# Performance work log

Hardware: AMD Instinct MI355X
Metric: run time of the kernel (lower is better)

Reference implementation:

```python
import jax, jax.numpy as jnp
import numpy as np

B, S, D_MODEL, D_STATE = 4, 2048, 2048, 64
C = 8.0
SURPRISE_TEMP = 1.0
RMS_EPS = 1e-6


def _l2norm(x, eps=1e-12):
    # F.normalize(dim=-1): x / max(||x||_2, eps)
    n = jnp.sqrt(jnp.sum(x * x, axis=-1, keepdims=True))
    return x / jnp.maximum(n, eps)


def setup_inputs() -> dict:
    key = jax.random.key(0)
    ks = jax.random.split(key, 9)
    std = 0.02
    return {
        "x": jax.random.normal(ks[0], (B, S, D_MODEL), dtype=jnp.float32),
        "Wk": jax.random.normal(ks[1], (D_STATE, D_MODEL), dtype=jnp.float32) * std,
        "Wv": jax.random.normal(ks[2], (D_STATE, D_MODEL), dtype=jnp.float32) * std,
        "Wq": jax.random.normal(ks[3], (D_STATE, D_MODEL), dtype=jnp.float32) * std,
        "Wa_w": jax.random.normal(ks[4], (D_STATE, D_MODEL), dtype=jnp.float32) * std,
        "Wa_b": jnp.zeros((D_STATE,), dtype=jnp.float32),
        "lam": jax.random.uniform(ks[5], (D_STATE,), dtype=jnp.float32, minval=4.0, maxval=9.0),
        "norm_w": jnp.ones((D_STATE,), dtype=jnp.float32),
        "Wo": jax.random.normal(ks[6], (D_MODEL, D_STATE), dtype=jnp.float32) * std,
    }


def reference(x, Wk, Wv, Wq, Wa_w, Wa_b, lam, norm_w, Wo):
    b, s, _ = x.shape
    d = Wk.shape[0]
    # projections
    k = _l2norm(x @ Wk.T)                    # [B,S,d]
    v = x @ Wv.T                             # [B,S,d]
    q = _l2norm(x @ Wq.T)                    # [B,S,d]
    r = jax.nn.sigmoid(x @ Wa_w.T + Wa_b)    # [B,S,d]
    log_a = jnp.log(jax.nn.sigmoid(lam) + 1e-8)
    alpha = jnp.exp(C * r * log_a)           # [B,S,d]

    def step(H, inp):
        # H: [B, d_k, d_v]; inp tensors: [B, d]
        k_t, v_t, q_t, a_t = inp
        pred = jnp.einsum("bk,bkv->bv", q_t, H)
        err = jnp.sum((v_t - pred) ** 2, axis=-1, keepdims=True)   # [B,1]
        surprise = jax.nn.sigmoid(err / (SURPRISE_TEMP + 1e-6))    # [B,1]
        kH = jnp.einsum("bk,bkv->bv", k_t, H)
        # delta = k (x) v - k (x) (k^T H) = k (x) (v - kH)
        delta = k_t[:, :, None] * (v_t - kH)[:, None, :]           # [B,d,d]
        a = a_t[:, :, None]                                        # gate over k-dim rows
        H = a * H + (1.0 - a) * (surprise[:, :, None] * delta)
        y_t = jnp.einsum("bk,bkv->bv", q_t, H)
        return H, y_t

    H0 = jnp.zeros((b, d, d), dtype=x.dtype)
    xs = (
        jnp.swapaxes(k, 0, 1),
        jnp.swapaxes(v, 0, 1),
        jnp.swapaxes(q, 0, 1),
        jnp.swapaxes(alpha, 0, 1),
    )
    _, ys = jax.lax.scan(step, H0, xs)       # ys: [S,B,d]
    y = jnp.swapaxes(ys, 0, 1)               # [B,S,d]

    # RMSNorm (computed in fp32, cast back)
    yf = y.astype(jnp.float32)
    yn = yf * jax.lax.rsqrt(jnp.mean(yf * yf, axis=-1, keepdims=True) + RMS_EPS)
    yn = (yn * norm_w).astype(y.dtype)

    return yn @ Wo.T                          # [B,S,d_model]
```

## Files before the change

kernel.cpp:

```cpp
#include <hip/hip_runtime.h>
#include <hip/hip_bf16.h>
#include <math.h>

#define B_ 4
#define S_ 2048
#define DM_ 2048

__device__ __forceinline__ float wave_reduce_add_f32(float x) {
  float t;
  t = __int_as_float(__builtin_amdgcn_update_dpp(0, __float_as_int(x), 0x111, 0xf, 0xf, true)); x += t;
  t = __int_as_float(__builtin_amdgcn_update_dpp(0, __float_as_int(x), 0x112, 0xf, 0xf, true)); x += t;
  t = __int_as_float(__builtin_amdgcn_update_dpp(0, __float_as_int(x), 0x114, 0xf, 0xf, true)); x += t;
  t = __int_as_float(__builtin_amdgcn_update_dpp(0, __float_as_int(x), 0x118, 0xf, 0xf, true)); x += t;
  t = __int_as_float(__builtin_amdgcn_update_dpp(0, __float_as_int(x), 0x142, 0xa, 0xf, true)); x += t;
  t = __int_as_float(__builtin_amdgcn_update_dpp(0, __float_as_int(x), 0x143, 0xc, 0xf, true)); x += t;
  return __int_as_float(__builtin_amdgcn_readlane(__float_as_int(x), 63));
}

__global__ __launch_bounds__(256) void k_proj(
    const float* __restrict__ x, const float* __restrict__ Wk,
    const float* __restrict__ Wv, const float* __restrict__ Wq,
    const float* __restrict__ Wa, const float* __restrict__ Wab,
    const float* __restrict__ lam, float* __restrict__ proj)
{
  __shared__ __align__(16) float xs[16 * 40];
  __shared__ __align__(16) float ws[32 * 260];
  const int tid = threadIdx.x;
  const int r0  = blockIdx.x * 16;
  const int ct  = tid & 63;
  const int rt  = tid >> 6;
  float acc[4][4];
  #pragma unroll
  for (int r = 0; r < 4; r++) { acc[r][0] = 0.f; acc[r][1] = 0.f; acc[r][2] = 0.f; acc[r][3] = 0.f; }

  const int sg = tid >> 3;
  const int sm = tid & 7;
  const float* wbase[4] = {Wk, Wv, Wq, Wa};

  for (int k0 = 0; k0 < DM_; k0 += 32) {
    if (tid < 128) {
      const int rr = tid >> 3;
      const int ko = (tid & 7) << 2;
      float4 xv = *(const float4*)(x + (size_t)(r0 + rr) * DM_ + k0 + ko);
      *(float4*)(xs + rr * 40 + ko) = xv;
    }
    #pragma unroll
    for (int p = 0; p < 8; p++) {
      const int c = sg + p * 32;
      const float* wb = wbase[p >> 1];
      const int cc = c - (p >> 1) * 64;
      float4 wv = *(const float4*)(wb + (size_t)cc * DM_ + k0 + sm * 4);
      ws[(sm * 4 + 0) * 260 + c] = wv.x;
      ws[(sm * 4 + 1) * 260 + c] = wv.y;
      ws[(sm * 4 + 2) * 260 + c] = wv.z;
      ws[(sm * 4 + 3) * 260 + c] = wv.w;
    }
    __syncthreads();
    #pragma unroll
    for (int kq = 0; kq < 8; kq++) {
      float4 xv[4];
      #pragma unroll
      for (int r = 0; r < 4; r++) xv[r] = *(const float4*)(xs + (rt * 4 + r) * 40 + kq * 4);
      #pragma unroll
      for (int i = 0; i < 4; i++) {
        const int kk = kq * 4 + i;
        float wv0 = ws[kk * 260 + ct];
        float wv1 = ws[kk * 260 + ct + 64];
        float wv2 = ws[kk * 260 + ct + 128];
        float wv3 = ws[kk * 260 + ct + 192];
        #pragma unroll
        for (int r = 0; r < 4; r++) {
          float xr = (i == 0) ? xv[r].x : (i == 1) ? xv[r].y : (i == 2) ? xv[r].z : xv[r].w;
          acc[r][0] = fmaf(xr, wv0, acc[r][0]);
          acc[r][1] = fmaf(xr, wv1, acc[r][1]);
          acc[r][2] = fmaf(xr, wv2, acc[r][2]);
          acc[r][3] = fmaf(xr, wv3, acc[r][3]);
        }
      }
    }
    __syncthreads();
  }
  float lamv = lam[ct];
  float la = logf(1.f / (1.f + expf(-lamv)) + 1e-8f);
  float bv = Wab[ct];
  #pragma unroll
  for (int r = 0; r < 4; r++) {
    float nk = wave_reduce_add_f32(acc[r][0] * acc[r][0]);
    float nq = wave_reduce_add_f32(acc[r][2] * acc[r][2]);
    nk = fmaxf(sqrtf(nk), 1e-12f);
    nq = fmaxf(sqrtf(nq), 1e-12f);
    float pre = acc[r][3] + bv;
    float rr_ = 1.f / (1.f + expf(-pre));
    float al  = expf(8.f * rr_ * la);
    float* pr = proj + (size_t)(r0 + rt * 4 + r) * 256;
    pr[ct]        = acc[r][0] / nk;
    pr[64 + ct]   = acc[r][1];
    pr[128 + ct]  = acc[r][2] / nq;
    pr[192 + ct]  = al;
  }
}

__global__ __launch_bounds__(256) void k_scan(const float* __restrict__ proj,
                                              float* __restrict__ ypart)
{
  __shared__ __align__(16) float inv[2][256];
  __shared__ __align__(16) float red[2][2][4][64];
  const int b    = blockIdx.x;
  const int tid  = threadIdx.x;
  const int w    = tid >> 6;
  const int lane = tid & 63;
  const int kb   = w * 16;
  float H[16];
  #pragma unroll
  for (int j = 0; j < 16; j++) H[j] = 0.f;
  const float* pb = proj + (size_t)b * S_ * 256;
  float* yb = ypart + (size_t)b * S_ * 256;
  float pf0 = pb[tid];
  float pf1 = pb[256 + tid];
  for (int t = 0; t < S_; t++) {
    const int pp = t & 1;
    inv[pp][tid] = pf0;
    pf0 = pf1;
    pf1 = (t + 2 < S_) ? pb[(size_t)(t + 2) * 256 + tid] : 0.f;
    __syncthreads();
    float k_[16], q_[16], a_[16];
    #pragma unroll
    for (int jq = 0; jq < 4; jq++) {
      *(float4*)(k_ + jq * 4) = *(const float4*)(&inv[pp][kb + jq * 4]);
      *(float4*)(q_ + jq * 4) = *(const float4*)(&inv[pp][128 + kb + jq * 4]);
      *(float4*)(a_ + jq * 4) = *(const float4*)(&inv[pp][192 + kb + jq * 4]);
    }
    float vv = inv[pp][64 + lane];
    float pred_p = 0.f, kH_p = 0.f;
    #pragma unroll
    for (int j = 0; j < 16; j++) {
      pred_p = fmaf(q_[j], H[j], pred_p);
      kH_p   = fmaf(k_[j], H[j], kH_p);
    }
    red[pp][0][w][lane] = pred_p;
    red[pp][1][w][lane] = kH_p;
    __syncthreads();
    float pred = (red[pp][0][0][lane] + red[pp][0][1][lane]) + (red[pp][0][2][lane] + red[pp][0][3][lane]);
    float kH   = (red[pp][1][0][lane] + red[pp][1][1][lane]) + (red[pp][1][2][lane] + red[pp][1][3][lane]);
    float d = vv - pred;
    float e = wave_reduce_add_f32(d * d);
    float s = 1.f / (1.f + expf(-e * (1.f / 1.000001f)));
    float g = s * (vv - kH);
    float yp = 0.f;
    #pragma unroll
    for (int j = 0; j < 16; j++) {
      H[j] = fmaf(a_[j], H[j], (1.f - a_[j]) * k_[j] * g);
      yp = fmaf(q_[j], H[j], yp);
    }
    yb[(size_t)t * 256 + w * 64 + lane] = yp;
  }
}

__global__ __launch_bounds__(256) void k_trans(const float* __restrict__ Wo,
                                               float* __restrict__ WoT) {
  int i = blockIdx.x * 256 + threadIdx.x;
  int d = i >> 11;
  int c = i & 2047;
  WoT[i] = Wo[(size_t)c * 64 + d];
}

__global__ __launch_bounds__(256) void k_out(const float* __restrict__ ypart,
    const float* __restrict__ norm_w, const float* __restrict__ WoT,
    float* __restrict__ out)
{
  __shared__ __align__(16) float yn[16 * 64];
  const int tid = threadIdx.x;
  const int r0  = blockIdx.x * 16;
  const int c0  = blockIdx.y * 512;
  {
    const int r = tid >> 4;
    const int d = (tid & 15) * 4;
    const float* yp = ypart + (size_t)(r0 + r) * 256;
    float4 y0 = *(const float4*)(yp + d);
    float4 y1 = *(const float4*)(yp + 64 + d);
    float4 y2 = *(const float4*)(yp + 128 + d);
    float4 y3 = *(const float4*)(yp + 192 + d);
    float yx = y0.x + y1.x + y2.x + y3.x;
    float yy = y0.y + y1.y + y2.y + y3.y;
    float yz = y0.z + y1.z + y2.z + y3.z;
    float yw = y0.w + y1.w + y2.w + y3.w;
    float sq = yx * yx + yy * yy + yz * yz + yw * yw;
    sq += __shfl_xor(sq, 1, 64);
    sq += __shfl_xor(sq, 2, 64);
    sq += __shfl_xor(sq, 4, 64);
    sq += __shfl_xor(sq, 8, 64);
    float rms = rsqrtf(sq * (1.f / 64.f) + 1e-6f);
    float4 nw = *(const float4*)(norm_w + d);
    yn[r * 64 + d + 0] = yx * rms * nw.x;
    yn[r * 64 + d + 1] = yy * rms * nw.y;
    yn[r * 64 + d + 2] = yz * rms * nw.z;
    yn[r * 64 + d + 3] = yw * rms * nw.w;
  }
  __syncthreads();
  const int ctq = tid & 127;
  const int rt  = tid >> 7;
  float acc[8][4];
  #pragma unroll
  for (int r = 0; r < 8; r++) { acc[r][0] = 0.f; acc[r][1] = 0.f; acc[r][2] = 0.f; acc[r][3] = 0.f; }
  #pragma unroll 8
  for (int d = 0; d < 64; d++) {
    float4 wv = *(const float4*)(WoT + (size_t)d * 2048 + c0 + ctq * 4);
    #pragma unroll
    for (int r = 0; r < 8; r++) {
      float yv = yn[(rt * 8 + r) * 64 + d];
      acc[r][0] = fmaf(yv, wv.x, acc[r][0]);
      acc[r][1] = fmaf(yv, wv.y, acc[r][1]);
      acc[r][2] = fmaf(yv, wv.z, acc[r][2]);
      acc[r][3] = fmaf(yv, wv.w, acc[r][3]);
    }
  }
  #pragma unroll
  for (int r = 0; r < 8; r++) {
    float4 o; o.x = acc[r][0]; o.y = acc[r][1]; o.z = acc[r][2]; o.w = acc[r][3];
    *(float4*)(out + (size_t)(r0 + rt * 8 + r) * 2048 + c0 + ctq * 4) = o;
  }
}

extern "C" void kernel_launch(void* const* d_in, const int* in_sizes, int n_in,
                              void* d_out, int out_size, void* d_ws, size_t ws_size,
                              hipStream_t stream) {
  const float* x   = (const float*)d_in[0];
  const float* Wk  = (const float*)d_in[1];
  const float* Wv  = (const float*)d_in[2];
  const float* Wq  = (const float*)d_in[3];
  const float* Wa  = (const float*)d_in[4];
  const float* Wab = (const float*)d_in[5];
  const float* lam = (const float*)d_in[6];
  const float* nw  = (const float*)d_in[7];
  const float* Wo  = (const float*)d_in[8];
  float* out = (float*)d_out;

  float* wsf   = (float*)d_ws;
  float* proj  = wsf;
  float* ypart = wsf + 2097152;
  float* WoT   = wsf + 4194304;

  k_trans<<<dim3(512), dim3(256), 0, stream>>>(Wo, WoT);
  k_proj <<<dim3(512), dim3(256), 0, stream>>>(x, Wk, Wv, Wq, Wa, Wab, lam, proj);
  k_scan <<<dim3(4),   dim3(256), 0, stream>>>(proj, ypart);
  k_out  <<<dim3(512, 4), dim3(256), 0, stream>>>(ypart, nw, WoT, out);
}
```

Measured before the change: 1.440 ms.

## Prefetch scan inputs directly into registers and drop one barrier per step

The scan kernel now loads each timestep's k, q, alpha, (1-alpha)*k and v straight from global memory into registers, two steps ahead with a ping-pong register set. This removes the shared-memory staging buffer and one __syncthreads per step. The projection kernel precomputes (1-alpha)*k into a wider row stride, and the reduction uses a transposed shared layout so each lane reads its partials with a single float4 load, plus a raw s_barrier and a fast reciprocal/exp. The cost is more register pressure, a larger workspace and redundant global loads of the same row across waves.

Measured after the change: 1.911 ms. 32.7% more time.

```diff
diff --git a/kernel.cpp b/kernel.cpp
--- a/kernel.cpp
+++ b/kernel.cpp
@@ -5,6 +5,7 @@
 #define B_ 4
 #define S_ 2048
 #define DM_ 2048
+#define PROJ_STRIDE 320
 
 __device__ __forceinline__ float wave_reduce_add_f32(float x) {
   float t;
@@ -92,67 +93,87 @@
     float pre = acc[r][3] + bv;
     float rr_ = 1.f / (1.f + expf(-pre));
     float al  = expf(8.f * rr_ * la);
-    float* pr = proj + (size_t)(r0 + rt * 4 + r) * 256;
-    pr[ct]        = acc[r][0] / nk;
+    float kn  = acc[r][0] / nk;
+    float* pr = proj + (size_t)(r0 + rt * 4 + r) * PROJ_STRIDE;
+    pr[ct]        = kn;
     pr[64 + ct]   = acc[r][1];
     pr[128 + ct]  = acc[r][2] / nq;
     pr[192 + ct]  = al;
-  }
+    pr[256 + ct]  = (1.f - al) * kn;
+  }
+}
+
+__device__ __forceinline__ void load_row(const float* __restrict__ r,
+    float4 K[4], float4 Q[4], float4 A[4], float4 W[4], float& V,
+    int w, int lane) {
+  const float4* r4 = (const float4*)r;
+  const int o = w * 4;
+  #pragma unroll
+  for (int i = 0; i < 4; i++) {
+    K[i] = r4[o + i];
+    Q[i] = r4[32 + o + i];
+    A[i] = r4[48 + o + i];
+    W[i] = r4[64 + o + i];
+  }
+  V = r[64 + lane];
+}
+
+__device__ __forceinline__ void scan_step(int t, const float* __restrict__ pb,
+    float* __restrict__ yb, float H[16],
+    float4 K[4], float4 Q[4], float4 A[4], float4 W[4], float& V,
+    float (*sp)[4], float (*sk)[4], int w, int lane) {
+  float pA = 0.f, pB = 0.f, kA = 0.f, kB = 0.f;
+  #pragma unroll
+  for (int jq = 0; jq < 4; jq++) {
+    pA = fmaf(Q[jq].x, H[4 * jq + 0], pA); kA = fmaf(K[jq].x, H[4 * jq + 0], kA);
+    pB = fmaf(Q[jq].y, H[4 * jq + 1], pB); kB = fmaf(K[jq].y, H[4 * jq + 1], kB);
+    pA = fmaf(Q[jq].z, H[4 * jq + 2], pA); kA = fmaf(K[jq].z, H[4 * jq + 2], kA);
+    pB = fmaf(Q[jq].w, H[4 * jq + 3], pB); kB = fmaf(K[jq].w, H[4 * jq + 3], kB);
+  }
+  sp[lane][w] = pA + pB;
+  sk[lane][w] = kA + kB;
+  asm volatile("s_waitcnt lgkmcnt(0)\n\ts_barrier" ::: "memory");
+  float4 P  = *(const float4*)sp[lane];
+  float4 Kp = *(const float4*)sk[lane];
+  float pred = (P.x + P.y) + (P.z + P.w);
+  float kh   = (Kp.x + Kp.y) + (Kp.z + Kp.w);
+  float d = V - pred;
+  float e = wave_reduce_add_f32(d * d);
+  float s = __builtin_amdgcn_rcpf(1.f + __expf(-e * (1.f / 1.000001f)));
+  float g = s * (V - kh);
+  float yA = 0.f, yB = 0.f;
+  #pragma unroll
+  for (int jq = 0; jq < 4; jq++) {
+    H[4 * jq + 0] = fmaf(A[jq].x, H[4 * jq + 0], W[jq].x * g); yA = fmaf(Q[jq].x, H[4 * jq + 0], yA);
+    H[4 * jq + 1] = fmaf(A[jq].y, H[4 * jq + 1], W[jq].y * g); yB = fmaf(Q[jq].y, H[4 * jq + 1], yB);
+    H[4 * jq + 2] = fmaf(A[jq].z, H[4 * jq + 2], W[jq].z * g); yA = fmaf(Q[jq].z, H[4 * jq + 2], yA);
+    H[4 * jq + 3] = fmaf(A[jq].w, H[4 * jq + 3], W[jq].w * g); yB = fmaf(Q[jq].w, H[4 * jq + 3], yB);
+  }
+  yb[(size_t)t * 256 + w * 64 + lane] = yA + yB;
+  const int tp = t + 2;
+  if (tp < S_) load_row(pb + (size_t)tp * PROJ_STRIDE, K, Q, A, W, V, w, lane);
 }
 
 __global__ __launch_bounds__(256) void k_scan(const float* __restrict__ proj,
                                               float* __restrict__ ypart)
 {
-  __shared__ __align__(16) float inv[2][256];
-  __shared__ __align__(16) float red[2][2][4][64];
+  __shared__ __align__(16) float sp0[64][4], sk0[64][4], sp1[64][4], sk1[64][4];
   const int b    = blockIdx.x;
   const int tid  = threadIdx.x;
   const int w    = tid >> 6;
   const int lane = tid & 63;
-  const int kb   = w * 16;
+  const float* pb = proj + (size_t)b * S_ * PROJ_STRIDE;
+  float* yb = ypart + (size_t)b * S_ * 256;
   float H[16];
   #pragma unroll
   for (int j = 0; j < 16; j++) H[j] = 0.f;
-  const float* pb = proj + (size_t)b * S_ * 256;
-  float* yb = ypart + (size_t)b * S_ * 256;
-  float pf0 = pb[tid];
-  float pf1 = pb[256 + tid];
-  for (int t = 0; t < S_; t++) {
-    const int pp = t & 1;
-    inv[pp][tid] = pf0;
-    pf0 = pf1;
-    pf1 = (t + 2 < S_) ? pb[(size_t)(t + 2) * 256 + tid] : 0.f;
-    __syncthreads();
-    float k_[16], q_[16], a_[16];
-    #pragma unroll
-    for (int jq = 0; jq < 4; jq++) {
-      *(float4*)(k_ + jq * 4) = *(const float4*)(&inv[pp][kb + jq * 4]);
-      *(float4*)(q_ + jq * 4) = *(const float4*)(&inv[pp][128 + kb + jq * 4]);
-      *(float4*)(a_ + jq * 4) = *(const float4*)(&inv[pp][192 + kb + jq * 4]);
-    }
-    float vv = inv[pp][64 + lane];
-    float pred_p = 0.f, kH_p = 0.f;
-    #pragma unroll
-    for (int j = 0; j < 16; j++) {
-      pred_p = fmaf(q_[j], H[j], pred_p);
-      kH_p   = fmaf(k_[j], H[j], kH_p);
-    }
-    red[pp][0][w][lane] = pred_p;
-    red[pp][1][w][lane] = kH_p;
-    __syncthreads();
-    float pred = (red[pp][0][0][lane] + red[pp][0][1][lane]) + (red[pp][0][2][lane] + red[pp][0][3][lane]);
-    float kH   = (red[pp][1][0][lane] + red[pp][1][1][lane]) + (red[pp][1][2][lane] + red[pp][1][3][lane]);
-    float d = vv - pred;
-    float e = wave_reduce_add_f32(d * d);
-    float s = 1.f / (1.f + expf(-e * (1.f / 1.000001f)));
-    float g = s * (vv - kH);
-    float yp = 0.f;
-    #pragma unroll
-    for (int j = 0; j < 16; j++) {
-      H[j] = fmaf(a_[j], H[j], (1.f - a_[j]) * k_[j] * g);
-      yp = fmaf(q_[j], H[j], yp);
-    }
-    yb[(size_t)t * 256 + w * 64 + lane] = yp;
+  float4 KA[4], QA[4], AA[4], WA[4]; float VA;
+  float4 KB[4], QB[4], AB[4], WB[4]; float VB;
+  load_row(pb,               KA, QA, AA, WA, VA, w, lane);
+  load_row(pb + PROJ_STRIDE, KB, QB, AB, WB, VB, w, lane);
+  for (int t = 0; t < S_; t += 2) {
+    scan_step(t,     pb, yb, H, KA, QA, AA, WA, VA, sp0, sk0, w, lane);
+    scan_step(t + 1, pb, yb, H, KB, QB, AB, WB, VB, sp1, sk1, w, lane);
   }
 }
 
@@ -237,8 +258,8 @@
 
   float* wsf   = (float*)d_ws;
   float* proj  = wsf;
-  float* ypart = wsf + 2097152;
-  float* WoT   = wsf + 4194304;
+  float* ypart = wsf + 2621440;
+  float* WoT   = wsf + 4718592;
 
   k_trans<<<dim3(512), dim3(256), 0, stream>>>(Wo, WoT);
   k_proj <<<dim3(512), dim3(256), 0, stream>>>(x, Wk, Wv, Wq, Wa, Wab, lam, proj);
```

## Restructure scan with 16-slot LDS ring, precomputed gate terms, one barrier per step

Applied to the files above, without the earlier changes.

The projection kernel now also precomputes (1-a)*k, q*a and the scalar q·((1-a)k) per timestep. This lets the scan compute y from the old state plus a correction term, so the y dot product no longer waits on the state update. The scan stages inputs through a 16-step shared-memory ring that is refilled every 8 steps, and prefetches the next step's operands into registers. That leaves one barrier per step instead of two, and a fast exp2/rcp sigmoid is used. The cost is a larger projection buffer (416 floats per row), more register pressure, and clamped tail loads.

New measurement: 1.717 ms. 1.19x slower.

```diff
diff --git a/kernel.cpp b/kernel.cpp
--- a/kernel.cpp
+++ b/kernel.cpp
@@ -5,6 +5,8 @@
 #define B_ 4
 #define S_ 2048
 #define DM_ 2048
+#define PST 416
+#define PST4 104
 
 __device__ __forceinline__ float wave_reduce_add_f32(float x) {
   float t;
@@ -92,67 +94,126 @@
     float pre = acc[r][3] + bv;
     float rr_ = 1.f / (1.f + expf(-pre));
     float al  = expf(8.f * rr_ * la);
-    float* pr = proj + (size_t)(r0 + rt * 4 + r) * 256;
-    pr[ct]        = acc[r][0] / nk;
+    float kn  = acc[r][0] / nk;
+    float qn  = acc[r][2] / nq;
+    float w_  = (1.f - al) * kn;
+    float qa_ = qn * al;
+    float qw  = wave_reduce_add_f32(qn * w_);
+    float* pr = proj + (size_t)(r0 + rt * 4 + r) * PST;
+    pr[ct]        = kn;
     pr[64 + ct]   = acc[r][1];
-    pr[128 + ct]  = acc[r][2] / nq;
+    pr[128 + ct]  = qn;
     pr[192 + ct]  = al;
-  }
-}
-
-__global__ __launch_bounds__(256) void k_scan(const float* __restrict__ proj,
-                                              float* __restrict__ ypart)
+    pr[256 + ct]  = w_;
+    pr[320 + ct]  = qa_;
+    if (ct == 0) pr[384] = qw;
+  }
+}
+
+struct InSet { float4 K[4], Q[4], QA[4]; float V; };
+
+__device__ __forceinline__ void prefetch_in(const float* __restrict__ slot,
+                                            InSet& s, int w, int lane) {
+  const float4* s4 = (const float4*)slot;
+  const int o = w * 4;
+  #pragma unroll
+  for (int i = 0; i < 4; i++) {
+    s.K[i]  = s4[o + i];
+    s.Q[i]  = s4[32 + o + i];
+    s.QA[i] = s4[80 + o + i];
+  }
+  s.V = slot[64 + lane];
+}
+
+__device__ __forceinline__ void refill(int t, float* __restrict__ ring,
+    float4 P[4], const float4* __restrict__ pb4, int tid) {
+  float4* dst = (float4*)(ring + ((t + 8) & 8) * PST);
+  dst[tid] = P[0]; dst[tid + 256] = P[1]; dst[tid + 512] = P[2];
+  if (tid < 64) dst[tid + 768] = P[3];
+  const int lim = S_ * PST4 - 1;
+  const int base = (t + 16) * PST4;
+  P[0] = pb4[min(base + tid,       lim)];
+  P[1] = pb4[min(base + tid + 256, lim)];
+  P[2] = pb4[min(base + tid + 512, lim)];
+  if (tid < 64) P[3] = pb4[min(base + tid + 768, lim)];
+}
+
+__device__ __forceinline__ void scan_step(int t, const float* __restrict__ ring,
+    float2* __restrict__ xchp, float* __restrict__ yb, float H[16],
+    InSet& cur, InSet& nxt, int w, int lane, float qwSel)
 {
-  __shared__ __align__(16) float inv[2][256];
-  __shared__ __align__(16) float red[2][2][4][64];
-  const int b    = blockIdx.x;
-  const int tid  = threadIdx.x;
-  const int w    = tid >> 6;
-  const int lane = tid & 63;
-  const int kb   = w * 16;
+  const float* slotc = ring + (t & 15) * PST;
+  const float* slotn = ring + ((t + 1) & 15) * PST;
+  float4 Av[4], Wv[4];
+  {
+    const float4* sc4 = (const float4*)slotc;
+    const int o = w * 4;
+    #pragma unroll
+    for (int i = 0; i < 4; i++) { Av[i] = sc4[48 + o + i]; Wv[i] = sc4[64 + o + i]; }
+  }
+  float qw = slotc[384];
+  prefetch_in(slotn, nxt, w, lane);
+  float pA = 0.f, pB = 0.f, kA = 0.f, kB = 0.f, yA = 0.f, yB = 0.f;
+  #pragma unroll
+  for (int j = 0; j < 4; j++) {
+    pA = fmaf(cur.Q[j].x, H[4*j+0], pA); kA = fmaf(cur.K[j].x, H[4*j+0], kA); yA = fmaf(cur.QA[j].x, H[4*j+0], yA);
+    pB = fmaf(cur.Q[j].y, H[4*j+1], pB); kB = fmaf(cur.K[j].y, H[4*j+1], kB); yB = fmaf(cur.QA[j].y, H[4*j+1], yB);
+    pA = fmaf(cur.Q[j].z, H[4*j+2], pA); kA = fmaf(cur.K[j].z, H[4*j+2], kA); yA = fmaf(cur.QA[j].z, H[4*j+2], yA);
+    pB = fmaf(cur.Q[j].w, H[4*j+3], pB); kB = fmaf(cur.K[j].w, H[4*j+3], kB); yB = fmaf(cur.QA[j].w, H[4*j+3], yB);
+  }
+  xchp[w * 64 + lane] = make_float2(pA + pB, kA + kB);
+  asm volatile("s_waitcnt lgkmcnt(0)\n\ts_barrier" ::: "memory");
+  float2 x0 = xchp[lane], x1 = xchp[64 + lane], x2 = xchp[128 + lane], x3 = xchp[192 + lane];
+  float pred = (x0.x + x1.x) + (x2.x + x3.x);
+  float kh   = (x0.y + x1.y) + (x2.y + x3.y);
+  float d = cur.V - pred;
+  float e = wave_reduce_add_f32(d * d);
+  float s = __builtin_amdgcn_rcpf(1.f + __builtin_amdgcn_exp2f(e * -1.4426936f));
+  float g = s * (cur.V - kh);
+  yb[(size_t)t * 256 + w * 64 + lane] = (yA + yB) + qwSel * (qw * g);
+  #pragma unroll
+  for (int j = 0; j < 4; j++) {
+    H[4*j+0] = fmaf(Av[j].x, H[4*j+0], Wv[j].x * g);
+    H[4*j+1] = fmaf(Av[j].y, H[4*j+1], Wv[j].y * g);
+    H[4*j+2] = fmaf(Av[j].z, H[4*j+2], Wv[j].z * g);
+    H[4*j+3] = fmaf(Av[j].w, H[4*j+3], Wv[j].w * g);
+  }
+}
+
+__global__ __launch_bounds__(256, 1) void k_scan(const float* __restrict__ proj,
+                                                 float* __restrict__ ypart)
+{
+  __shared__ __align__(16) float ring[16 * PST];
+  __shared__ __align__(16) float2 xch[2][4 * 64];
+  const int b = blockIdx.x, tid = threadIdx.x;
+  const int w = tid >> 6, lane = tid & 63;
+  const float* pb = proj + (size_t)b * S_ * PST;
+  const float4* pb4 = (const float4*)pb;
+  float* yb = ypart + (size_t)b * S_ * 256;
   float H[16];
   #pragma unroll
   for (int j = 0; j < 16; j++) H[j] = 0.f;
-  const float* pb = proj + (size_t)b * S_ * 256;
-  float* yb = ypart + (size_t)b * S_ * 256;
-  float pf0 = pb[tid];
-  float pf1 = pb[256 + tid];
-  for (int t = 0; t < S_; t++) {
-    const int pp = t & 1;
-    inv[pp][tid] = pf0;
-    pf0 = pf1;
-    pf1 = (t + 2 < S_) ? pb[(size_t)(t + 2) * 256 + tid] : 0.f;
-    __syncthreads();
-    float k_[16], q_[16], a_[16];
-    #pragma unroll
-    for (int jq = 0; jq < 4; jq++) {
-      *(float4*)(k_ + jq * 4) = *(const float4*)(&inv[pp][kb + jq * 4]);
-      *(float4*)(q_ + jq * 4) = *(const float4*)(&inv[pp][128 + kb + jq * 4]);
-      *(float4*)(a_ + jq * 4) = *(const float4*)(&inv[pp][192 + kb + jq * 4]);
-    }
-    float vv = inv[pp][64 + lane];
-    float pred_p = 0.f, kH_p = 0.f;
-    #pragma unroll
-    for (int j = 0; j < 16; j++) {
-      pred_p = fmaf(q_[j], H[j], pred_p);
-      kH_p   = fmaf(k_[j], H[j], kH_p);
-    }
-    red[pp][0][w][lane] = pred_p;
-    red[pp][1][w][lane] = kH_p;
-    __syncthreads();
-    float pred = (red[pp][0][0][lane] + red[pp][0][1][lane]) + (red[pp][0][2][lane] + red[pp][0][3][lane]);
-    float kH   = (red[pp][1][0][lane] + red[pp][1][1][lane]) + (red[pp][1][2][lane] + red[pp][1][3][lane]);
-    float d = vv - pred;
-    float e = wave_reduce_add_f32(d * d);
-    float s = 1.f / (1.f + expf(-e * (1.f / 1.000001f)));
-    float g = s * (vv - kH);
-    float yp = 0.f;
-    #pragma unroll
-    for (int j = 0; j < 16; j++) {
-      H[j] = fmaf(a_[j], H[j], (1.f - a_[j]) * k_[j] * g);
-      yp = fmaf(q_[j], H[j], yp);
-    }
-    yb[(size_t)t * 256 + w * 64 + lane] = yp;
+  float4 P[4];
+  P[0] = pb4[tid]; P[1] = pb4[tid + 256]; P[2] = pb4[tid + 512];
+  if (tid < 64) P[3] = pb4[tid + 768];
+  {
+    float4* dst = (float4*)ring;
+    dst[tid] = P[0]; dst[tid + 256] = P[1]; dst[tid + 512] = P[2];
+    if (tid < 64) dst[tid + 768] = P[3];
+  }
+  {
+    const int base = 8 * PST4;
+    P[0] = pb4[base + tid]; P[1] = pb4[base + tid + 256]; P[2] = pb4[base + tid + 512];
+    if (tid < 64) P[3] = pb4[base + tid + 768];
+  }
+  __syncthreads();
+  const float qwSel = (w == 0) ? 1.f : 0.f;
+  InSet inA, inB;
+  prefetch_in(ring, inA, w, lane);
+  for (int t = 0; t < S_; t += 2) {
+    if ((t & 7) == 0) refill(t, ring, P, pb4, tid);
+    scan_step(t,     ring, xch[0], yb, H, inA, inB, w, lane, qwSel);
+    scan_step(t + 1, ring, xch[1], yb, H, inB, inA, w, lane, qwSel);
   }
 }
 
@@ -237,8 +298,8 @@
 
   float* wsf   = (float*)d_ws;
   float* proj  = wsf;
-  float* ypart = wsf + 2097152;
-  float* WoT   = wsf + 4194304;
+  float* ypart = wsf + 3407872;
+  float* WoT   = wsf + 5505024;
 
   k_trans<<<dim3(512), dim3(256), 0, stream>>>(Wo, WoT);
   k_proj <<<dim3(512), dim3(256), 0, stream>>>(x, Wk, Wv, Wq, Wa, Wab, lam, proj);
```

## Chunk the surprise-gated delta scan into 16-step blocks with cumulative-decay algebra

Applied to the files above, without the earlier changes.

Replaces the per-timestep scan, which needed two block barriers per step, with a chunked formulation. Each chunk of 16 steps rescales q, k and the write weights by cumulative decay products. Inter-chunk contributions are then computed as small matrix products against the stored state, and only the scalar surprise recurrence stays sequential, done within a wave using precomputed intra-chunk coefficients. The scan now writes the fully reduced y (64 per row) instead of four partial sums, so the output kernel reads a quarter of the data. Dividing by cumulative decay products risks underflow or precision loss when decays are small, and the kernel uses much more shared memory and more redundant arithmetic.

New measurement: 1.378 ms. 4.4% less time.

```diff
diff --git a/kernel.cpp b/kernel.cpp
--- a/kernel.cpp
+++ b/kernel.cpp
@@ -2,9 +2,10 @@
 #include <hip/hip_bf16.h>
 #include <math.h>
 
-#define B_ 4
 #define S_ 2048
 #define DM_ 2048
+#define CK 16
+#define NCH (S_ / CK)
 
 __device__ __forceinline__ float wave_reduce_add_f32(float x) {
   float t;
@@ -100,59 +101,186 @@
   }
 }
 
-__global__ __launch_bounds__(256) void k_scan(const float* __restrict__ proj,
-                                              float* __restrict__ ypart)
+__global__ __launch_bounds__(256, 1) void k_scan(const float* __restrict__ proj,
+                                                 float* __restrict__ ypart)
 {
-  __shared__ __align__(16) float inv[2][256];
-  __shared__ __align__(16) float red[2][2][4][64];
-  const int b    = blockIdx.x;
-  const int tid  = threadIdx.x;
-  const int w    = tid >> 6;
-  const int lane = tid & 63;
-  const int kb   = w * 16;
+  __shared__ __align__(16) float slab[CK * 256];
+  __shared__ __align__(16) float qt [CK * 68];
+  __shared__ __align__(16) float kt2[CK * 68];
+  __shared__ __align__(16) float wt [CK * 68];
+  __shared__ __align__(16) float Pt [CK * 64];
+  __shared__ __align__(16) float H0t[64 * 64];
+  __shared__ __align__(16) float QKb[CK * 64 * 2];
+  __shared__ __align__(16) float Yb [CK * 64];
+  __shared__ __align__(16) float QCm[256], KCm[256], YCm[256];
+
+  const int b = blockIdx.x, tid = threadIdx.x;
+  const int w = tid >> 6, lane = tid & 63;
+  const float* pb = proj + (size_t)b * S_ * 256;
+  float* yb = ypart + (size_t)b * S_ * 64;
+
   float H[16];
   #pragma unroll
   for (int j = 0; j < 16; j++) H[j] = 0.f;
-  const float* pb = proj + (size_t)b * S_ * 256;
-  float* yb = ypart + (size_t)b * S_ * 256;
-  float pf0 = pb[tid];
-  float pf1 = pb[256 + tid];
-  for (int t = 0; t < S_; t++) {
-    const int pp = t & 1;
-    inv[pp][tid] = pf0;
-    pf0 = pf1;
-    pf1 = (t + 2 < S_) ? pb[(size_t)(t + 2) * 256 + tid] : 0.f;
-    __syncthreads();
-    float k_[16], q_[16], a_[16];
-    #pragma unroll
-    for (int jq = 0; jq < 4; jq++) {
-      *(float4*)(k_ + jq * 4) = *(const float4*)(&inv[pp][kb + jq * 4]);
-      *(float4*)(q_ + jq * 4) = *(const float4*)(&inv[pp][128 + kb + jq * 4]);
-      *(float4*)(a_ + jq * 4) = *(const float4*)(&inv[pp][192 + kb + jq * 4]);
-    }
-    float vv = inv[pp][64 + lane];
-    float pred_p = 0.f, kH_p = 0.f;
-    #pragma unroll
-    for (int j = 0; j < 16; j++) {
-      pred_p = fmaf(q_[j], H[j], pred_p);
-      kH_p   = fmaf(k_[j], H[j], kH_p);
-    }
-    red[pp][0][w][lane] = pred_p;
-    red[pp][1][w][lane] = kH_p;
-    __syncthreads();
-    float pred = (red[pp][0][0][lane] + red[pp][0][1][lane]) + (red[pp][0][2][lane] + red[pp][0][3][lane]);
-    float kH   = (red[pp][1][0][lane] + red[pp][1][1][lane]) + (red[pp][1][2][lane] + red[pp][1][3][lane]);
-    float d = vv - pred;
-    float e = wave_reduce_add_f32(d * d);
-    float s = 1.f / (1.f + expf(-e * (1.f / 1.000001f)));
-    float g = s * (vv - kH);
-    float yp = 0.f;
-    #pragma unroll
-    for (int j = 0; j < 16; j++) {
-      H[j] = fmaf(a_[j], H[j], (1.f - a_[j]) * k_[j] * g);
-      yp = fmaf(q_[j], H[j], yp);
-    }
-    yb[(size_t)t * 256 + w * 64 + lane] = yp;
+  #pragma unroll
+  for (int i = 0; i < 16; i++) H0t[i * 256 + tid] = 0.f;
+  float pf[16];
+  #pragma unroll
+  for (int i = 0; i < 16; i++) pf[i] = pb[i * 256 + tid];
+
+  for (int n = 0; n < NCH; n++) {
+    const int t0 = n << 4;
+    #pragma unroll
+    for (int i = 0; i < 16; i++) slab[i * 256 + tid] = pf[i];
+    if (tid >= 192) {
+      const int k = tid - 192;
+      float p = 1.f;
+      #pragma unroll
+      for (int s = 0; s < 16; s++) { p *= pf[s]; Pt[s * 64 + k] = p; }
+    }
+    #pragma unroll
+    for (int i = 0; i < 16; i++) {
+      int tt = t0 + 16 + i; tt = tt < S_ ? tt : S_ - 1;
+      pf[i] = pb[(size_t)tt * 256 + tid];
+    }
+    __syncthreads();
+    {
+      const int s  = tid >> 4;
+      const int kq = (tid & 15) << 2;
+      float4 qv = *(const float4*)&slab[s * 256 + 128 + kq];
+      float4 av = *(const float4*)&slab[s * 256 + 192 + kq];
+      float4 kv = *(const float4*)&slab[s * 256 + 0   + kq];
+      float4 P1 = *(const float4*)&Pt[s * 64 + kq];
+      float4 P0;
+      if (s == 0) { P0.x = P0.y = P0.z = P0.w = 1.f; }
+      else        { P0 = *(const float4*)&Pt[(s - 1) * 64 + kq]; }
+      float4 qtv, ktv, wtv;
+      qtv.x = qv.x * P0.x; qtv.y = qv.y * P0.y; qtv.z = qv.z * P0.z; qtv.w = qv.w * P0.w;
+      ktv.x = kv.x * P0.x; ktv.y = kv.y * P0.y; ktv.z = kv.z * P0.z; ktv.w = kv.w * P0.w;
+      wtv.x = (1.f - av.x) * kv.x / P1.x;
+      wtv.y = (1.f - av.y) * kv.y / P1.y;
+      wtv.z = (1.f - av.z) * kv.z / P1.z;
+      wtv.w = (1.f - av.w) * kv.w / P1.w;
+      *(float4*)&qt [s * 68 + kq] = qtv;
+      *(float4*)&kt2[s * 68 + kq] = ktv;
+      *(float4*)&wt [s * 68 + kq] = wtv;
+    }
+    __syncthreads();
+    {
+      float aq[4] = {0.f, 0.f, 0.f, 0.f};
+      float ak[4] = {0.f, 0.f, 0.f, 0.f};
+      float ay[4] = {0.f, 0.f, 0.f, 0.f};
+      #pragma unroll
+      for (int kb = 0; kb < 16; kb++) {
+        float h0 = H0t[(kb * 4 + 0) * 64 + lane];
+        float h1 = H0t[(kb * 4 + 1) * 64 + lane];
+        float h2 = H0t[(kb * 4 + 2) * 64 + lane];
+        float h3 = H0t[(kb * 4 + 3) * 64 + lane];
+        #pragma unroll
+        for (int i = 0; i < 4; i++) {
+          const int t = w + (i << 2);
+          float4 qv = *(const float4*)&qt [t * 68 + kb * 4];
+          float4 kv = *(const float4*)&kt2[t * 68 + kb * 4];
+          float4 av = *(const float4*)&slab[t * 256 + 192 + kb * 4];
+          aq[i] = fmaf(qv.x, h0, fmaf(qv.y, h1, fmaf(qv.z, h2, fmaf(qv.w, h3, aq[i]))));
+          ak[i] = fmaf(kv.x, h0, fmaf(kv.y, h1, fmaf(kv.z, h2, fmaf(kv.w, h3, ak[i]))));
+          ay[i] = fmaf(qv.x * av.x, h0, fmaf(qv.y * av.y, h1,
+                  fmaf(qv.z * av.z, h2, fmaf(qv.w * av.w, h3, ay[i]))));
+        }
+      }
+      #pragma unroll
+      for (int i = 0; i < 4; i++) {
+        const int t = w + (i << 2);
+        *(float2*)&QKb[(t * 64 + lane) * 2] = make_float2(aq[i], ak[i]);
+        Yb[t * 64 + lane] = ay[i];
+      }
+    }
+    {
+      const int t = tid >> 4, s = tid & 15;
+      float accq = 0.f, acck = 0.f, accy = 0.f;
+      #pragma unroll
+      for (int kb = 0; kb < 16; kb++) {
+        float4 wv = *(const float4*)&wt [s * 68 + kb * 4];
+        float4 qv = *(const float4*)&qt [t * 68 + kb * 4];
+        float4 kv = *(const float4*)&kt2[t * 68 + kb * 4];
+        float4 av = *(const float4*)&slab[t * 256 + 192 + kb * 4];
+        accq = fmaf(qv.x, wv.x, fmaf(qv.y, wv.y, fmaf(qv.z, wv.z, fmaf(qv.w, wv.w, accq))));
+        acck = fmaf(kv.x, wv.x, fmaf(kv.y, wv.y, fmaf(kv.z, wv.z, fmaf(kv.w, wv.w, acck))));
+        accy = fmaf(qv.x * av.x, wv.x, fmaf(qv.y * av.y, wv.y,
+               fmaf(qv.z * av.z, wv.z, fmaf(qv.w * av.w, wv.w, accy))));
+      }
+      QCm[tid] = accq; KCm[tid] = acck; YCm[tid] = accy;
+    }
+    __syncthreads();
+    float g[16];
+    #pragma unroll
+    for (int t = 0; t < 16; t++) {
+      float qrow[16], krow[16];
+      *(float4*)&qrow[0]  = *(const float4*)&QCm[t * 16 + 0];
+      *(float4*)&qrow[4]  = *(const float4*)&QCm[t * 16 + 4];
+      *(float4*)&qrow[8]  = *(const float4*)&QCm[t * 16 + 8];
+      *(float4*)&qrow[12] = *(const float4*)&QCm[t * 16 + 12];
+      *(float4*)&krow[0]  = *(const float4*)&KCm[t * 16 + 0];
+      *(float4*)&krow[4]  = *(const float4*)&KCm[t * 16 + 4];
+      *(float4*)&krow[8]  = *(const float4*)&KCm[t * 16 + 8];
+      *(float4*)&krow[12] = *(const float4*)&KCm[t * 16 + 12];
+      float2 qk = *(const float2*)&QKb[(t * 64 + lane) * 2];
+      float V = slab[t * 256 + 64 + lane];
+      float pred = qk.x, kh = qk.y;
+      #pragma unroll
+      for (int s = 0; s < t; s++) {
+        pred = fmaf(qrow[s], g[s], pred);
+        kh   = fmaf(krow[s], g[s], kh);
+      }
+      float d = V - pred;
+      float e = wave_reduce_add_f32(d * d);
+      float sur = __builtin_amdgcn_rcpf(1.f + __builtin_amdgcn_exp2f(e * -1.4426936f));
+      g[t] = sur * (V - kh);
+    }
+    #pragma unroll
+    for (int s = 0; s < 16; s++) {
+      float4 w0 = *(const float4*)&wt[s * 68 + (w << 4) + 0];
+      float4 w1 = *(const float4*)&wt[s * 68 + (w << 4) + 4];
+      float4 w2 = *(const float4*)&wt[s * 68 + (w << 4) + 8];
+      float4 w3 = *(const float4*)&wt[s * 68 + (w << 4) + 12];
+      H[0]  = fmaf(w0.x, g[s], H[0]);  H[1]  = fmaf(w0.y, g[s], H[1]);
+      H[2]  = fmaf(w0.z, g[s], H[2]);  H[3]  = fmaf(w0.w, g[s], H[3]);
+      H[4]  = fmaf(w1.x, g[s], H[4]);  H[5]  = fmaf(w1.y, g[s], H[5]);
+      H[6]  = fmaf(w1.z, g[s], H[6]);  H[7]  = fmaf(w1.w, g[s], H[7]);
+      H[8]  = fmaf(w2.x, g[s], H[8]);  H[9]  = fmaf(w2.y, g[s], H[9]);
+      H[10] = fmaf(w2.z, g[s], H[10]); H[11] = fmaf(w2.w, g[s], H[11]);
+      H[12] = fmaf(w3.x, g[s], H[12]); H[13] = fmaf(w3.y, g[s], H[13]);
+      H[14] = fmaf(w3.z, g[s], H[14]); H[15] = fmaf(w3.w, g[s], H[15]);
+    }
+    {
+      float4 p0 = *(const float4*)&Pt[15 * 64 + (w << 4) + 0];
+      float4 p1 = *(const float4*)&Pt[15 * 64 + (w << 4) + 4];
+      float4 p2 = *(const float4*)&Pt[15 * 64 + (w << 4) + 8];
+      float4 p3 = *(const float4*)&Pt[15 * 64 + (w << 4) + 12];
+      H[0]  *= p0.x; H[1]  *= p0.y; H[2]  *= p0.z; H[3]  *= p0.w;
+      H[4]  *= p1.x; H[5]  *= p1.y; H[6]  *= p1.z; H[7]  *= p1.w;
+      H[8]  *= p2.x; H[9]  *= p2.y; H[10] *= p2.z; H[11] *= p2.w;
+      H[12] *= p3.x; H[13] *= p3.y; H[14] *= p3.z; H[15] *= p3.w;
+      #pragma unroll
+      for (int j = 0; j < 16; j++) H0t[((w << 4) + j) * 64 + lane] = H[j];
+    }
+    #pragma unroll
+    for (int i = 0; i < 4; i++) {
+      const int t = w + (i << 2);
+      float yrow[16];
+      *(float4*)&yrow[0]  = *(const float4*)&YCm[t * 16 + 0];
+      *(float4*)&yrow[4]  = *(const float4*)&YCm[t * 16 + 4];
+      *(float4*)&yrow[8]  = *(const float4*)&YCm[t * 16 + 8];
+      *(float4*)&yrow[12] = *(const float4*)&YCm[t * 16 + 12];
+      float y = Yb[t * 64 + lane];
+      #pragma unroll
+      for (int s = 0; s < 16; s++) {
+        float c = (s <= t) ? yrow[s] : 0.f;
+        y = fmaf(c, g[s], y);
+      }
+      yb[(size_t)(t0 + t) * 64 + lane] = y;
+    }
+    __syncthreads();
   }
 }
 
@@ -175,26 +303,19 @@
   {
     const int r = tid >> 4;
     const int d = (tid & 15) * 4;
-    const float* yp = ypart + (size_t)(r0 + r) * 256;
-    float4 y0 = *(const float4*)(yp + d);
-    float4 y1 = *(const float4*)(yp + 64 + d);
-    float4 y2 = *(const float4*)(yp + 128 + d);
-    float4 y3 = *(const float4*)(yp + 192 + d);
-    float yx = y0.x + y1.x + y2.x + y3.x;
-    float yy = y0.y + y1.y + y2.y + y3.y;
-    float yz = y0.z + y1.z + y2.z + y3.z;
-    float yw = y0.w + y1.w + y2.w + y3.w;
-    float sq = yx * yx + yy * yy + yz * yz + yw * yw;
+    const float* yp = ypart + (size_t)(r0 + r) * 64;
+    float4 yv = *(const float4*)(yp + d);
+    float sq = yv.x * yv.x + yv.y * yv.y + yv.z * yv.z + yv.w * yv.w;
     sq += __shfl_xor(sq, 1, 64);
     sq += __shfl_xor(sq, 2, 64);
     sq += __shfl_xor(sq, 4, 64);
     sq += __shfl_xor(sq, 8, 64);
     float rms = rsqrtf(sq * (1.f / 64.f) + 1e-6f);
     float4 nw = *(const float4*)(norm_w + d);
-    yn[r * 64 + d + 0] = yx * rms * nw.x;
-    yn[r * 64 + d + 1] = yy * rms * nw.y;
-    yn[r * 64 + d + 2] = yz * rms * nw.z;
-    yn[r * 64 + d + 3] = yw * rms * nw.w;
+    yn[r * 64 + d + 0] = yv.x * rms * nw.x;
+    yn[r * 64 + d + 1] = yv.y * rms * nw.y;
+    yn[r * 64 + d + 2] = yv.z * rms * nw.z;
+    yn[r * 64 + d + 3] = yv.w * rms * nw.w;
   }
   __syncthreads();
   const int ctq = tid & 127;
@@ -238,7 +359,7 @@
   float* wsf   = (float*)d_ws;
   float* proj  = wsf;
   float* ypart = wsf + 2097152;
-  float* WoT   = wsf + 4194304;
+  float* WoT   = wsf + 2621440;
 
   k_trans<<<dim3(512), dim3(256), 0, stream>>>(Wo, WoT);
   k_proj <<<dim3(512), dim3(256), 0, stream>>>(x, Wk, Wv, Wq, Wa, Wab, lam, proj);
```
